# Kernel tuning notes

Hardware: AMD Instinct MI355X
Metric: run time of the kernel (lower is better)

The kernel has to match this reference:

```python
import jax, jax.numpy as jnp
import numpy as np

B, T, D, H = 4, 3072, 1024, 16
HD = D // H

def setup_inputs() -> dict:
    key = jax.random.key(0)
    ks = jax.random.split(key, 7)
    s = 1.0 / np.sqrt(D)
    x = jax.random.normal(ks[0], (B, T, D), dtype=jnp.float32)
    Wq = jax.random.normal(ks[1], (D, D), dtype=jnp.float32) * s
    Wk = jax.random.normal(ks[2], (D, D), dtype=jnp.float32) * s
    Wv = jax.random.normal(ks[3], (D, D), dtype=jnp.float32) * s
    Wo = jax.random.normal(ks[4], (D, D), dtype=jnp.float32) * s
    bo = jnp.zeros((D,), dtype=jnp.float32)
    Wconv = jax.random.normal(ks[5], (D, D, 3), dtype=jnp.float32) * (1.0 / np.sqrt(3 * D))  # (out, in, kw)
    return {"x": x, "Wq": Wq, "Wk": Wk, "Wv": Wv, "Wo": Wo, "bo": bo, "Wconv": Wconv}

def reference(x, Wq, Wk, Wv, Wo, bo, Wconv):
    b, t, d = x.shape
    # stride-3 conv pooling of K/V stream (Conv1d(D, D, 3, stride=3, bias=False))
    kc = jax.lax.conv_general_dilated(
        x.transpose(0, 2, 1), Wconv, window_strides=(3,), padding='VALID',
        dimension_numbers=('NCH', 'OIH', 'NCH')).transpose(0, 2, 1)  # (B, T//3, D)
    k_tmp = jnp.concatenate([x[:, :1, :], kc], axis=1)  # (B, Tk, D)
    tk = k_tmp.shape[1]
    # comparison-based bias mask: masked where 3*k_idx >= q_idx + 0.001
    q_idx = jnp.arange(t, dtype=jnp.float32)
    k_idx = jnp.arange(tk, dtype=jnp.float32)
    mask = (k_idx[None, :] * 3.0 >= q_idx[:, None] + 0.001).astype(x.dtype)  # (T, Tk)
    # projections (torch Linear: y = x @ W.T)
    q = x @ Wq.T
    k = k_tmp @ Wk.T
    v = k_tmp @ Wv.T
    q = q.reshape(b, t, H, HD).transpose(0, 2, 1, 3)   # (B, H, T, HD)
    k = k.reshape(b, tk, H, HD).transpose(0, 2, 1, 3)  # (B, H, Tk, HD)
    v = v.reshape(b, tk, H, HD).transpose(0, 2, 1, 3)
    scores = jnp.einsum('bhqd,bhkd->bhqk', q, k) * (HD ** -0.5)
    scores = scores + mask * jnp.asarray(-1e9, dtype=x.dtype)
    p = jax.nn.softmax(scores, axis=-1)  # dropout is identity in eval (p=0)
    o = jnp.einsum('bhqk,bhkd->bhqd', p, v)
    o = o.transpose(0, 2, 1, 3).reshape(b, t, d)
    return o @ Wo.T + bo
```

## Files before the change

kernel.cpp:

```cpp
#include <hip/hip_runtime.h>
#include <hip/hip_bf16.h>
#include <cstdint>
#include <cstddef>

typedef __attribute__((ext_vector_type(8))) __bf16 bf16x8;
typedef __attribute__((ext_vector_type(4))) __bf16 bf16x4;
typedef __attribute__((ext_vector_type(4))) float  floatx4;

#define MFMA16x16x32(a, b, c) __builtin_amdgcn_mfma_f32_16x16x32_bf16((a), (b), (c), 0, 0, 0)

#define ATTN_SC 0.18033688011112042f

__device__ __forceinline__ void gload_lds16(const void* g, void* l) {
  __builtin_amdgcn_global_load_lds((const __attribute__((address_space(1))) void*)g,
                                   (__attribute__((address_space(3))) void*)l,
                                   16, 0, 0);
}


__global__ void prep_kernel(const float* __restrict__ x,
                            const float* __restrict__ Wq, const float* __restrict__ Wk,
                            const float* __restrict__ Wv, const float* __restrict__ Wo,
                            const float* __restrict__ Wconv,
                            __bf16* __restrict__ xb,
                            __bf16* __restrict__ wqb, __bf16* __restrict__ wkb,
                            __bf16* __restrict__ wvb, __bf16* __restrict__ wob,
                            __bf16* __restrict__ wc2, __bf16* __restrict__ ktmp) {
  const int bid = blockIdx.x, tid = threadIdx.x;
  if (bid < 4096) {
    const int which = bid >> 10;
    const float* src = (which == 0) ? Wq : (which == 1) ? Wk : (which == 2) ? Wv : Wo;
    __bf16* dst = (which == 0) ? wqb : (which == 1) ? wkb : (which == 2) ? wvb : wob;
    const int i = (bid & 1023) * 256 + tid;
    floatx4 v = *(const floatx4*)(src + (size_t)i * 4);
    bf16x4 o; o[0] = (__bf16)v[0]; o[1] = (__bf16)v[1]; o[2] = (__bf16)v[2]; o[3] = (__bf16)v[3];
    *(bf16x4*)(dst + (size_t)i * 4) = o;
  } else if (bid < 5120) {
    const int t = (bid - 4096) * 256 + tid;
    const int o = t >> 8, c = t & 255;
    const float* base = Wconv + (size_t)o * 3072 + c * 12;
    float f[12];
    *(floatx4*)(f)     = *(const floatx4*)(base);
    *(floatx4*)(f + 4) = *(const floatx4*)(base + 4);
    *(floatx4*)(f + 8) = *(const floatx4*)(base + 8);
#pragma unroll
    for (int kw = 0; kw < 3; ++kw) {
      bf16x4 q;
#pragma unroll
      for (int j = 0; j < 4; ++j) q[j] = (__bf16)f[3 * j + kw];
      *(bf16x4*)(wc2 + (size_t)o * 3072 + kw * 1024 + c * 4) = q;
    }
  } else if (bid < 5136) {
    const int i = (bid - 5120) * 256 + tid;
    const int b = i >> 10, c = i & 1023;
    ktmp[(size_t)b * 1025 * 1024 + c] = (__bf16)x[(size_t)b * 3072 * 1024 + c];
  } else {
    const int i = (bid - 5136) * 256 + tid;
    floatx4 v = *(const floatx4*)(x + (size_t)i * 4);
    bf16x4 o; o[0] = (__bf16)v[0]; o[1] = (__bf16)v[1]; o[2] = (__bf16)v[2]; o[3] = (__bf16)v[3];
    *(bf16x4*)(xb + (size_t)i * 4) = o;
  }
}

__global__ void vtrans_kernel(const __bf16* __restrict__ V, __bf16* __restrict__ Vt) {
  __shared__ __attribute__((aligned(16))) __bf16 tile[64][72];
  const int tid = threadIdx.x;
  const int bh = blockIdx.y;
  const int b = bh >> 4, h = bh & 15;
  const int t0 = blockIdx.x * 64;
  const int r = tid >> 3, s = tid & 7;
#pragma unroll
  for (int p = 0; p < 2; ++p) {
    const int t = p * 32 + r;
    bf16x8 v = *(const bf16x8*)(V + ((size_t)(b * 1025 + t0 + t)) * 1024 + h * 64 + s * 8);
    *(bf16x8*)(&tile[t][s * 8]) = v;
  }
  __syncthreads();
#pragma unroll
  for (int p = 0; p < 2; ++p) {
    const int d = p * 32 + r;
    bf16x8 o;
#pragma unroll
    for (int e = 0; e < 8; ++e) o[e] = tile[s * 8 + e][d];
    *(bf16x8*)(Vt + ((size_t)bh * 64 + d) * 1024 + t0 + s * 8) = o;
  }
}


template <int MODE>
__device__ __forceinline__ void gemm8_body(
    const __bf16* __restrict__ A, const __bf16* __restrict__ Bw, void* __restrict__ Cout,
    const float* __restrict__ bias, int N, int K, int m0, int n0,
    __bf16* As, __bf16* Bs)
{
  const int tid  = threadIdx.x;
  const int wave = tid >> 6;
  const int lane = tid & 63;
  const int g    = lane >> 4;
  const int ln   = lane & 15;
  const int wr   = (wave >> 2) * 64;
  const int wc   = (wave & 3) * 64;

  const int prow = tid >> 3;
  const int pc   = tid & 7;
  const int ca   = pc ^ (prow & 7);
  const size_t aSrc  = (size_t)(m0 + prow + ((ca >> 2) << 6)) * K + ((ca & 3) << 3);
  const size_t bSrc0 = (size_t)(n0 + prow + ((ca >> 2) << 7)) * K + ((ca & 3) << 3);
  const size_t bSrc1 = bSrc0 + (size_t)64 * K;

  int aOff[4], bOff[4];
#pragma unroll
  for (int i = 0; i < 4; ++i) {
    const int ra = wr + i * 16 + ln;
    const int pr = ra & 63;
    const int c  = ((ra >> 6) << 2) + g;
    aOff[i] = pr * 64 + ((c ^ (pr & 7)) << 3);
  }
#pragma unroll
  for (int j = 0; j < 4; ++j) {
    const int rb = wc + j * 16 + ln;
    const int pr = rb & 127;
    const int c  = ((rb >> 7) << 2) + g;
    bOff[j] = pr * 64 + ((c ^ (pr & 7)) << 3);
  }

  floatx4 acc[4][4];
#pragma unroll
  for (int i = 0; i < 4; ++i)
#pragma unroll
    for (int j = 0; j < 4; ++j) { floatx4 z = {0.f, 0.f, 0.f, 0.f}; acc[i][j] = z; }

  __bf16* const ad0 = As + (tid << 3);
  __bf16* const bd0 = Bs + (tid << 3);

  auto STAGE = [&](int halfidx) {
    const int slot = halfidx & 3;
    const int koff = (halfidx >> 1) * 64 + ((halfidx & 1) << 5);
    gload_lds16(A  + aSrc  + koff, ad0 + (slot << 12));
    gload_lds16(Bw + bSrc0 + koff, bd0 + (slot << 13));
    gload_lds16(Bw + bSrc1 + koff, bd0 + (slot << 13) + 4096);
  };

  const int HT = K >> 5;

  STAGE(0); STAGE(1); STAGE(2);
  asm volatile("s_waitcnt vmcnt(6)" ::: "memory");
  __builtin_amdgcn_s_barrier();
  __builtin_amdgcn_sched_barrier(0);

  for (int h = 0; h < HT; ++h) {
    const int slot = h & 3;
    const __bf16* ah = As + (slot << 12);
    const __bf16* bh = Bs + (slot << 13);
    bf16x8 af[4], bf[4];
#pragma unroll
    for (int i = 0; i < 4; ++i) af[i] = *(const bf16x8*)(ah + aOff[i]);
#pragma unroll
    for (int j = 0; j < 4; ++j) bf[j] = *(const bf16x8*)(bh + bOff[j]);

    if (h + 3 < HT) STAGE(h + 3);

    if (h + 1 < HT) {
      if (h + 3 < HT)      { asm volatile("s_waitcnt vmcnt(6)" ::: "memory"); }
      else if (h + 2 < HT) { asm volatile("s_waitcnt vmcnt(3)" ::: "memory"); }
      else                 { asm volatile("s_waitcnt vmcnt(0)" ::: "memory"); }
      __builtin_amdgcn_s_barrier();
      __builtin_amdgcn_sched_barrier(0);
    }

    __builtin_amdgcn_s_setprio(1);
#pragma unroll
    for (int i = 0; i < 4; ++i)
#pragma unroll
      for (int j = 0; j < 4; ++j)
        acc[i][j] = MFMA16x16x32(af[i], bf[j], acc[i][j]);
    __builtin_amdgcn_s_setprio(0);

    if (h + 1 < HT) {
      __builtin_amdgcn_s_barrier();
      __builtin_amdgcn_sched_barrier(0);
    }
  }

#pragma unroll
  for (int j = 0; j < 4; ++j) {
    const int col = n0 + wc + j * 16 + ln;
    float bj = 0.f;
    if (MODE == 2) bj = bias[col];
#pragma unroll
    for (int i = 0; i < 4; ++i)
#pragma unroll
      for (int r = 0; r < 4; ++r) {
        const int row = m0 + wr + i * 16 + g * 4 + r;
        if (MODE == 2) {
          ((float*)Cout)[(size_t)row * N + col] = acc[i][j][r] + bj;
        } else if (MODE == 1) {
          const size_t orow = (size_t)(row >> 10) * 1025 + 1 + (row & 1023);
          ((__bf16*)Cout)[orow * 1024 + col] = (__bf16)acc[i][j][r];
        } else if (MODE == 4) {
          ((__bf16*)Cout)[(size_t)row * N + col] = (__bf16)(acc[i][j][r] * ATTN_SC);
        } else {
          ((__bf16*)Cout)[(size_t)row * N + col] = (__bf16)acc[i][j][r];
        }
      }
  }
}

__global__ __launch_bounds__(512, 2) void gemm_convq_kernel(
    const __bf16* __restrict__ xb, const __bf16* __restrict__ wc2,
    const __bf16* __restrict__ wqb, __bf16* __restrict__ ktmp, __bf16* __restrict__ qb)
{
  __shared__ __attribute__((aligned(16))) __bf16 As[16384];
  __shared__ __attribute__((aligned(16))) __bf16 Bs[32768];
  const int xcd = blockIdx.x & 7, s = blockIdx.x >> 3;
  if (s < 16) {
    const int id = xcd * 16 + s;
    gemm8_body<1>(xb, wc2, ktmp, nullptr, 1024, 3072, (id >> 2) * 128, (id & 3) * 256, As, Bs);
  } else {
    const int id = xcd * 48 + (s - 16);
    gemm8_body<4>(xb, wqb, qb, nullptr, 1024, 1024, (id >> 2) * 128, (id & 3) * 256, As, Bs);
  }
}

__global__ __launch_bounds__(512, 2) void gemm_kv_kernel(
    const __bf16* __restrict__ ktmp, const __bf16* __restrict__ wkb,
    const __bf16* __restrict__ wvb, __bf16* __restrict__ kb, __bf16* __restrict__ vb)
{
  __shared__ __attribute__((aligned(16))) __bf16 As[16384];
  __shared__ __attribute__((aligned(16))) __bf16 Bs[32768];
  const int id = (blockIdx.x & 7) * 33 + (blockIdx.x >> 3);
  const int p  = (id >= 132) ? 1 : 0;
  const int rest = id - p * 132;
  gemm8_body<0>(ktmp, p ? wvb : wkb, p ? vb : kb, nullptr, 1024, 1024,
                (rest >> 2) * 128, (rest & 3) * 256, As, Bs);
}

__global__ __launch_bounds__(512, 2) void gemm_o_kernel(
    const __bf16* __restrict__ ob, const __bf16* __restrict__ wob,
    float* __restrict__ out, const float* __restrict__ bo)
{
  __shared__ __attribute__((aligned(16))) __bf16 As[16384];
  __shared__ __attribute__((aligned(16))) __bf16 Bs[32768];
  const int id = (blockIdx.x & 7) * 48 + (blockIdx.x >> 3);
  gemm8_body<2>(ob, wob, out, bo, 1024, 1024, (id >> 2) * 128, (id & 3) * 256, As, Bs);
}


__global__ __launch_bounds__(256) void attn_kernel(
    const __bf16* __restrict__ Q, const __bf16* __restrict__ Kk,
    const __bf16* __restrict__ Vt, __bf16* __restrict__ O)
{
  __shared__ __attribute__((aligned(16))) __bf16 Kd[2][64 * 64];
  __shared__ __attribute__((aligned(16))) __bf16 Vd[2][64 * 64];
  __shared__ __attribute__((aligned(16))) __bf16 Ps[4][32 * 64];

  const int tid  = threadIdx.x;
  const int wave = tid >> 6;
  const int lane = tid & 63;
  const int g    = lane >> 4;
  const int ln   = lane & 15;

  const int l    = blockIdx.x;
  const int xcd  = l & 7;
  const int b    = xcd >> 1;
  const int rest = l >> 3;
  const int h    = rest & 15;
  const int qt   = ((11 - (rest >> 4)) << 1) | (xcd & 1);
  const int q0   = qt * 128 + wave * 32;

  const size_t qrow0 = (size_t)b * 3072 + q0;
  const size_t krow0 = (size_t)b * 1025;
  const size_t vtrow = ((size_t)(b * 16 + h)) * 64;
  const int hc = h * 64;
  const int sw = (ln & 7) << 3;
  __bf16* Pw = Ps[wave];

  const int srow = lane >> 3;
  const int scol = (lane & 7) * 8;

  auto stage = [&](int kt, int bb) {
    const int kb0 = kt * 64;
#pragma unroll
    for (int i = 0; i < 2; ++i) {
      const int rr = (wave * 2 + i) * 8 + srow;
      gload_lds16(Kk + (krow0 + kb0 + rr) * 1024 + hc + scol,
                  Kd[bb] + (size_t)rr * 64 + scol);
      gload_lds16(Vt + (vtrow + rr) * 1024 + kb0 + scol,
                  Vd[bb] + (size_t)rr * 64 + scol);
    }
  };

  bf16x8 qf[2][2];
#pragma unroll
  for (int i = 0; i < 2; ++i)
#pragma unroll
    for (int kc = 0; kc < 2; ++kc)
      qf[i][kc] = *(const bf16x8*)(Q + (qrow0 + i * 16 + ln) * 1024 + hc + kc * 32 + g * 8);

  floatx4 oacc[2][4];
  floatx4 oal[2];
#pragma unroll
  for (int i = 0; i < 2; ++i) {
    floatx4 z = {0.f, 0.f, 0.f, 0.f};
    oal[i] = z;
#pragma unroll
    for (int dt = 0; dt < 4; ++dt) oacc[i][dt] = z;
  }

  bf16x8 ones;
#pragma unroll
  for (int e = 0; e < 8; ++e) ones[e] = (__bf16)1.0f;

  const int nkt_blk = (((qt * 128 + 127) / 3) >> 6) + 1;
  const int nfull   = (q0 >= 189) ? ((q0 - 189) / 192 + 1) : 0;

  stage(0, 0);

  for (int kt = 0; kt < nkt_blk; ++kt) {
    const int bb = kt & 1;
    __syncthreads();
    if (kt + 1 < nkt_blk) stage(kt + 1, bb ^ 1);
    const int kb0 = kt * 64;
    const bool masked = (kt >= nfull);

    bf16x8 kf[4][2];
#pragma unroll
    for (int jk = 0; jk < 4; ++jk)
#pragma unroll
      for (int kc = 0; kc < 2; ++kc)
        kf[jk][kc] = *(const bf16x8*)(Kd[bb] + (jk * 16 + ln) * 64 + kc * 32 + g * 8);

#pragma unroll
    for (int jk = 0; jk < 4; ++jk)
#pragma unroll
      for (int i = 0; i < 2; ++i) {
        floatx4 s = {0.f, 0.f, 0.f, 0.f};
        s = MFMA16x16x32(kf[jk][0], qf[i][0], s);
        s = MFMA16x16x32(kf[jk][1], qf[i][1], s);
        float p[4];
#pragma unroll
        for (int r = 0; r < 4; ++r) {
          float e = __builtin_amdgcn_exp2f(s[r]);
          if (masked) {
            const int key = kb0 + jk * 16 + 4 * g + r;
            const int q   = q0 + i * 16 + ln;
            e = (3 * key <= q) ? e : 0.f;
          }
          p[r] = e;
        }
        bf16x4 pk;
        pk[0] = (__bf16)p[0]; pk[1] = (__bf16)p[1]; pk[2] = (__bf16)p[2]; pk[3] = (__bf16)p[3];
        *(bf16x4*)(Pw + (i * 16 + ln) * 64 + ((jk * 16 + 4 * g) ^ sw)) = pk;
      }

#pragma unroll
    for (int kc = 0; kc < 2; ++kc) {
      bf16x8 pf0 = *(const bf16x8*)(Pw + (ln) * 64      + ((kc * 32 + g * 8) ^ sw));
      bf16x8 pf1 = *(const bf16x8*)(Pw + (16 + ln) * 64 + ((kc * 32 + g * 8) ^ sw));
      oal[0] = MFMA16x16x32(ones, pf0, oal[0]);
      oal[1] = MFMA16x16x32(ones, pf1, oal[1]);
#pragma unroll
      for (int dt = 0; dt < 4; ++dt) {
        bf16x8 vf = *(const bf16x8*)(Vd[bb] + (dt * 16 + ln) * 64 + kc * 32 + g * 8);
        oacc[0][dt] = MFMA16x16x32(vf, pf0, oacc[0][dt]);
        oacc[1][dt] = MFMA16x16x32(vf, pf1, oacc[1][dt]);
      }
    }
  }

#pragma unroll
  for (int i = 0; i < 2; ++i) {
    const float inv = 1.0f / oal[i][0];
    const size_t row = qrow0 + i * 16 + ln;
#pragma unroll
    for (int dt = 0; dt < 4; ++dt) {
      bf16x4 o4;
#pragma unroll
      for (int r = 0; r < 4; ++r) o4[r] = (__bf16)(oacc[i][dt][r] * inv);
      *(bf16x4*)(O + row * 1024 + hc + dt * 16 + 4 * g) = o4;
    }
  }
}


extern "C" void kernel_launch(void* const* d_in, const int* in_sizes, int n_in,
                              void* d_out, int out_size, void* d_ws, size_t ws_size,
                              hipStream_t stream) {
  (void)in_sizes; (void)n_in; (void)out_size; (void)ws_size;
  const float* x     = (const float*)d_in[0];
  const float* Wq    = (const float*)d_in[1];
  const float* Wk    = (const float*)d_in[2];
  const float* Wv    = (const float*)d_in[3];
  const float* Wo    = (const float*)d_in[4];
  const float* bo    = (const float*)d_in[5];
  const float* Wconv = (const float*)d_in[6];

  char* ws = (char*)d_ws;
  const size_t SZ_XQ = (size_t)12288 * 1024 * 2;
  const size_t SZ_KT = (size_t)4224 * 1024 * 2;
  const size_t SZ_W  = (size_t)1024 * 1024 * 2;

  __bf16* xb   = (__bf16*)(ws);
  __bf16* qb   = (__bf16*)(ws + SZ_XQ);
  __bf16* ktmp = (__bf16*)(ws + 2 * SZ_XQ);
  __bf16* kb   = (__bf16*)(ws + 2 * SZ_XQ + SZ_KT);
  __bf16* vb   = (__bf16*)(ws + 2 * SZ_XQ + 2 * SZ_KT);
  __bf16* wqb  = (__bf16*)(ws + 2 * SZ_XQ + 3 * SZ_KT);
  __bf16* wkb  = (__bf16*)(ws + 2 * SZ_XQ + 3 * SZ_KT + SZ_W);
  __bf16* wvb  = (__bf16*)(ws + 2 * SZ_XQ + 3 * SZ_KT + 2 * SZ_W);
  __bf16* wob  = (__bf16*)(ws + 2 * SZ_XQ + 3 * SZ_KT + 3 * SZ_W);
  __bf16* wc2  = (__bf16*)(ws + 2 * SZ_XQ + 3 * SZ_KT + 4 * SZ_W);
  __bf16* vt   = xb;

  prep_kernel<<<dim3(17424), dim3(256), 0, stream>>>(x, Wq, Wk, Wv, Wo, Wconv,
                                                     xb, wqb, wkb, wvb, wob, wc2, ktmp);
  gemm_convq_kernel<<<dim3(512), dim3(512), 0, stream>>>(xb, wc2, wqb, ktmp, qb);
  gemm_kv_kernel<<<dim3(264), dim3(512), 0, stream>>>(ktmp, wkb, wvb, kb, vb);
  vtrans_kernel<<<dim3(16, 64), dim3(256), 0, stream>>>(vb, vt);
  attn_kernel<<<dim3(1536), dim3(256), 0, stream>>>(qb, kb, vt, qb);
  gemm_o_kernel<<<dim3(384), dim3(512), 0, stream>>>(qb, wob, (float*)d_out, bo);
}
```

Measured before the change: 341.4 us.

## Double-buffer LDS fragment reads in GEMM main loop to overlap with MFMA

Restructures the GEMM k-loop into a two-phase ping-pong. The next half-tile's A/B fragments are read from LDS into a second register set while MFMAs run on the current set. The loop also adds a fourth prefetch stage and needs one barrier per half-step instead of two. This is meant to hide LDS read latency behind matrix math, at the cost of more registers and tighter waitcnt and slot-reuse logic.

```diff
diff --git a/kernel.cpp b/kernel.cpp
--- a/kernel.cpp
+++ b/kernel.cpp
@@ -141,46 +141,67 @@
     gload_lds16(Bw + bSrc1 + koff, bd0 + (slot << 13) + 4096);
   };
 
+  bf16x8 afA[4], bfA[4], afB[4], bfB[4];
+
+#define READF(AF, BF, slot)                                                        \
+  {                                                                                \
+    const __bf16* ah_ = As + ((slot) << 12);                                       \
+    const __bf16* bh_ = Bs + ((slot) << 13);                                       \
+    _Pragma("unroll")                                                              \
+    for (int i_ = 0; i_ < 4; ++i_) AF[i_] = *(const bf16x8*)(ah_ + aOff[i_]);      \
+    _Pragma("unroll")                                                              \
+    for (int j_ = 0; j_ < 4; ++j_) BF[j_] = *(const bf16x8*)(bh_ + bOff[j_]);      \
+  }
+
+#define MFMAC(AF, BF)                                                              \
+  {                                                                                \
+    __builtin_amdgcn_s_setprio(1);                                                 \
+    _Pragma("unroll")                                                              \
+    for (int i_ = 0; i_ < 4; ++i_)                                                 \
+      _Pragma("unroll")                                                            \
+      for (int j_ = 0; j_ < 4; ++j_)                                               \
+        acc[i_][j_] = MFMA16x16x32(AF[i_], BF[j_], acc[i_][j_]);                   \
+    __builtin_amdgcn_s_setprio(0);                                                 \
+  }
+
+#define PHASE_WAIT(x)                                                              \
+  {                                                                                \
+    if ((x) + 4 < HT)      { asm volatile("s_waitcnt vmcnt(6) lgkmcnt(0)" ::: "memory"); } \
+    else if ((x) + 3 < HT) { asm volatile("s_waitcnt vmcnt(3) lgkmcnt(0)" ::: "memory"); } \
+    else                   { asm volatile("s_waitcnt vmcnt(0) lgkmcnt(0)" ::: "memory"); } \
+  }
+
   const int HT = K >> 5;
 
   STAGE(0); STAGE(1); STAGE(2);
   asm volatile("s_waitcnt vmcnt(6)" ::: "memory");
   __builtin_amdgcn_s_barrier();
   __builtin_amdgcn_sched_barrier(0);
-
-  for (int h = 0; h < HT; ++h) {
-    const int slot = h & 3;
-    const __bf16* ah = As + (slot << 12);
-    const __bf16* bh = Bs + (slot << 13);
-    bf16x8 af[4], bf[4];
-#pragma unroll
-    for (int i = 0; i < 4; ++i) af[i] = *(const bf16x8*)(ah + aOff[i]);
-#pragma unroll
-    for (int j = 0; j < 4; ++j) bf[j] = *(const bf16x8*)(bh + bOff[j]);
-
-    if (h + 3 < HT) STAGE(h + 3);
-
-    if (h + 1 < HT) {
-      if (h + 3 < HT)      { asm volatile("s_waitcnt vmcnt(6)" ::: "memory"); }
-      else if (h + 2 < HT) { asm volatile("s_waitcnt vmcnt(3)" ::: "memory"); }
-      else                 { asm volatile("s_waitcnt vmcnt(0)" ::: "memory"); }
-      __builtin_amdgcn_s_barrier();
-      __builtin_amdgcn_sched_barrier(0);
+  READF(afA, bfA, 0);
+  STAGE(3);
+  asm volatile("s_waitcnt vmcnt(6) lgkmcnt(0)" ::: "memory");
+
+  for (int h = 0; h < HT; h += 2) {
+    __builtin_amdgcn_s_barrier();
+    __builtin_amdgcn_sched_barrier(0);
+    READF(afB, bfB, (h + 1) & 3);
+    MFMAC(afA, bfA);
+    if (h + 4 < HT) STAGE(h + 4);
+    PHASE_WAIT(h);
+
+    __builtin_amdgcn_s_barrier();
+    __builtin_amdgcn_sched_barrier(0);
+    if (h + 2 < HT) READF(afA, bfA, (h + 2) & 3);
+    MFMAC(afB, bfB);
+    if (h + 2 < HT) {
+      if (h + 5 < HT) STAGE(h + 5);
+      PHASE_WAIT(h + 1);
     }
-
-    __builtin_amdgcn_s_setprio(1);
-#pragma unroll
-    for (int i = 0; i < 4; ++i)
-#pragma unroll
-      for (int j = 0; j < 4; ++j)
-        acc[i][j] = MFMA16x16x32(af[i], bf[j], acc[i][j]);
-    __builtin_amdgcn_s_setprio(0);
-
-    if (h + 1 < HT) {
-      __builtin_amdgcn_s_barrier();
-      __builtin_amdgcn_sched_barrier(0);
-    }
-  }
+  }
+
+#undef READF
+#undef MFMAC
+#undef PHASE_WAIT
 
 #pragma unroll
   for (int j = 0; j < 4; ++j) {
```

After: 344.8 us. No clear change (+1.0%).
